# Kernel tuning notes

Hardware: AMD Instinct MI355X
Metric: run time of the kernel (lower is better)

The kernel has to match this reference:

```python
import jax, jax.numpy as jnp
import numpy as np

B, N, PHY, C, HID, FC, L, E = 2, 8192, 2, 64, 64, 128, 3, 524288

def _ln(x, g, b, eps=1e-5):
    mu = jnp.mean(x, axis=-1, keepdims=True)
    var = jnp.mean((x - mu) ** 2, axis=-1, keepdims=True)
    return (x - mu) * jax.lax.rsqrt(var + eps) * g + b

def setup_inputs() -> dict:
    key = jax.random.key(0)
    ks = jax.random.split(key, 24)
    s = 1.0 / np.sqrt(C)
    inp = {
        'x': jax.random.normal(ks[0], (B, N, 5), jnp.float32),
        'edge_index': jax.random.randint(ks[1], (2, E), 0, B * N, jnp.int32),
        'fc0_w': jax.random.normal(ks[2], (C, 4), jnp.float32) * 0.5,
        'fc0_b': jnp.zeros((C,), jnp.float32),
        'ln0_g': jnp.ones((C,), jnp.float32),
        'ln0_b': jnp.zeros((C,), jnp.float32),
        'gg_fc1_w': jax.random.normal(ks[3], (L, HID, C), jnp.float32) * s,
        'gg_fc1_b': jnp.zeros((L, HID), jnp.float32),
        'gg_fc2_w': jax.random.normal(ks[4], (L, C, HID), jnp.float32) * s,
        'gg_fc2_b': jnp.zeros((L, C), jnp.float32),
        'gg_weight': jax.random.uniform(ks[5], (L, HID), jnp.float32) + 0.5,
        'gg_freq': jax.random.normal(ks[6], (L, PHY, HID), jnp.float32) * (2 * np.pi),
        'wc_w': jax.random.normal(ks[7], (L, C, C), jnp.float32) * s,
        'wc_b': jnp.zeros((L, C), jnp.float32),
        'ln_g': jnp.ones((L, C), jnp.float32),
        'ln_b': jnp.zeros((L, C), jnp.float32),
        'fc1_w': jax.random.normal(ks[8], (FC, C), jnp.float32) * s,
        'fc1_b': jnp.zeros((FC,), jnp.float32),
        'fc2_w': jax.random.normal(ks[9], (1, FC), jnp.float32) / np.sqrt(FC),
        'fc2_b': jnp.zeros((1,), jnp.float32),
    }
    return inp

def reference(x, edge_index, fc0_w, fc0_b, ln0_g, ln0_b, gg_fc1_w, gg_fc1_b,
              gg_fc2_w, gg_fc2_b, gg_weight, gg_freq, wc_w, wc_b, ln_g, ln_b,
              fc1_w, fc1_b, fc2_w, fc2_b):
    grid = x[:, :, 2:4]           # (B,N,PHY): columns in_dim-phy_dim .. -1
    gw = x[:, :, 4]               # (B,N) grid_weight
    feat = x[:, :, :4]            # (B,N,in_dim)
    src, dst = edge_index[0], edge_index[1]
    grid_f = grid.reshape(-1, PHY)
    gw_f = gw.reshape(-1)
    vec = grid_f[src] - grid_f[dst]                      # (E,PHY)
    dist2 = jnp.sum(vec * vec, axis=-1, keepdims=True)   # (E,1)
    wgt_src = gw_f[src][:, None]                          # (E,1)

    h = feat @ fc0_w.T + fc0_b                            # (B,N,C)
    h = _ln(h, ln0_g, ln0_b)
    for l in range(L):
        w = gg_weight[l]                                  # (HID,)
        gauss = jnp.sqrt((w / jnp.pi) ** PHY) * jnp.exp(-w * dist2)  # (E,HID)
        fourier = jnp.sin(vec @ gg_freq[l])               # (E,HID)
        morlet = gauss * fourier
        hl = h @ gg_fc1_w[l].T + gg_fc1_b[l]              # (B,N,HID)
        val = morlet * hl.reshape(-1, HID)[src] * wgt_src # (E,HID)
        agg = jax.ops.segment_sum(val, dst, num_segments=B * N)
        x1 = agg.reshape(B, N, HID) @ gg_fc2_w[l].T + gg_fc2_b[l]
        x2 = h @ wc_w[l].T + wc_b[l]                      # pointwise Conv1d
        h = _ln(x1 + x2, ln_g[l], ln_b[l])
        if l != L - 1:
            h = jax.nn.gelu(h, approximate=False)
    h = jax.nn.gelu(h @ fc1_w.T + fc1_b, approximate=False)
    return h @ fc2_w.T + fc2_b                            # (B,N,1)
```

## Files before the change

### kernel.cpp

```cpp
#include <hip/hip_runtime.h>
#include <hip/hip_bf16.h>

#define M_NODES 16384
#define E_EDGES 524288
#define ASTR 68

typedef short short8 __attribute__((ext_vector_type(8)));
typedef float f32x4 __attribute__((ext_vector_type(4)));
typedef unsigned int uint4v __attribute__((ext_vector_type(4)));

#define PK_W1 0
#define PK_WC 12288
#define PK_W2 24576
#define PK_FC1 36864
#define PK_TOTAL 45056

static __device__ __forceinline__ float wredsum(float v) {
#pragma unroll
  for (int o = 32; o > 0; o >>= 1) v += __shfl_xor(v, o, 64);
  return v;
}

static __device__ __forceinline__ float gelu_exact(float x) {
  return 0.5f * x * (1.0f + erff(x * 0.70710678118654752440f));
}

static __device__ __forceinline__ unsigned int bsplit(float x) {
  unsigned int u = __float_as_uint(x);
  unsigned int hb = (u + 0x7FFFu + ((u >> 16) & 1u)) >> 16;
  float hf = __uint_as_float(hb << 16);
  float r = x - hf;
  unsigned int v = __float_as_uint(r);
  unsigned int lb = (v + 0x7FFFu + ((v >> 16) & 1u)) >> 16;
  return (hb & 0xFFFFu) | (lb << 16);
}

struct Frag { short8 hi, lo; };

static __device__ __forceinline__ Frag load_afrag(const unsigned int* a) {
  uint4v u0 = *(const uint4v*)a;
  uint4v u1 = *(const uint4v*)(a + 4);
  Frag f;
#pragma unroll
  for (int j = 0; j < 4; ++j) {
    f.hi[j]     = (short)(u0[j] & 0xFFFFu);
    f.lo[j]     = (short)(u0[j] >> 16);
    f.hi[j + 4] = (short)(u1[j] & 0xFFFFu);
    f.lo[j + 4] = (short)(u1[j] >> 16);
  }
  return f;
}

static __device__ __forceinline__ Frag load_bfrag(const float* __restrict__ w) {
  float4 w0 = *(const float4*)w;
  float4 w1 = *(const float4*)(w + 4);
  float v[8] = {w0.x, w0.y, w0.z, w0.w, w1.x, w1.y, w1.z, w1.w};
  Frag f;
#pragma unroll
  for (int j = 0; j < 8; ++j) {
    unsigned int p = bsplit(v[j]);
    f.hi[j] = (short)(p & 0xFFFFu);
    f.lo[j] = (short)(p >> 16);
  }
  return f;
}

static __device__ __forceinline__ f32x4 mfma3(const Frag& a, const Frag& b, f32x4 c) {
  c = __builtin_amdgcn_mfma_f32_16x16x32_bf16(a.hi, b.hi, c, 0, 0, 0);
  c = __builtin_amdgcn_mfma_f32_16x16x32_bf16(a.lo, b.hi, c, 0, 0, 0);
  c = __builtin_amdgcn_mfma_f32_16x16x32_bf16(a.hi, b.lo, c, 0, 0, 0);
  return c;
}

static __device__ __forceinline__ Frag load_bpk(const short* __restrict__ P, int S, int n, int off) {
  Frag f;
  f.hi = *(const short8*)(P + n * 64 + off);
  f.lo = *(const short8*)(P + S + n * 64 + off);
  return f;
}

__global__ __launch_bounds__(256) void k_front(
    const float* __restrict__ x,
    const float* __restrict__ fc0_w, const float* __restrict__ fc0_b,
    const float* __restrict__ ln0_g, const float* __restrict__ ln0_b,
    const float* __restrict__ gg_fc1_w, const float* __restrict__ gg_fc1_b,
    const float* __restrict__ wc_w, const float* __restrict__ wc_b,
    const float* __restrict__ gg_fc2_w, const float* __restrict__ fc1_w,
    const int* __restrict__ ei, int* __restrict__ cnt, short* __restrict__ pk,
    float2* __restrict__ grid2, float* __restrict__ gwf,
    float* __restrict__ hl, float* __restrict__ x2T)
{
  __shared__ unsigned int A[16 * ASTR];
  const int bid = blockIdx.x;
  const int tid = threadIdx.x;

  if (bid >= 3072) {
    int i = (bid - 3072) * 256 + tid;
    float v = (i < PK_WC)  ? gg_fc1_w[i]
            : (i < PK_W2)  ? wc_w[i - PK_WC]
            : (i < PK_FC1) ? gg_fc2_w[i - PK_W2]
                           : fc1_w[i - PK_FC1];
    int mb, sz;
    if (i < PK_FC1) { mb = i & ~4095; sz = 4096; } else { mb = PK_FC1; sz = 8192; }
    int k = i - mb;
    unsigned int p = bsplit(v);
    pk[2 * mb + k]      = (short)(p & 0xFFFFu);
    pk[2 * mb + sz + k] = (short)(p >> 16);
    return;
  }
  if (bid >= 1024) {
    int e = (bid - 1024) * 256 + tid;
    atomicAdd(&cnt[ei[E_EDGES + e]], 1);
    return;
  }

  const int lane = tid & 63, w = tid >> 6;
  const int tilebase = bid * 16;

  float fw0 = fc0_w[lane * 4 + 0], fw1 = fc0_w[lane * 4 + 1];
  float fw2v = fc0_w[lane * 4 + 2], fw3 = fc0_w[lane * 4 + 3];
  float fb = fc0_b[lane], g0 = ln0_g[lane], bb0 = ln0_b[lane];

#pragma unroll
  for (int i = 0; i < 4; ++i) {
    int node = tilebase + 4 * w + i;
    float xv0 = x[node * 5 + 0], xv1 = x[node * 5 + 1], xv2 = x[node * 5 + 2];
    float xv3 = x[node * 5 + 3], xv4 = x[node * 5 + 4];
    float acc = fb + xv0 * fw0 + xv1 * fw1 + xv2 * fw2v + xv3 * fw3;
    float mean = wredsum(acc) * (1.0f / 64.0f);
    float d = acc - mean;
    float var = wredsum(d * d) * (1.0f / 64.0f);
    float hv = d * rsqrtf(var + 1e-5f) * g0 + bb0;
    A[(4 * w + i) * ASTR + lane] = bsplit(hv);
    if (lane == 0) { grid2[node] = make_float2(xv2, xv3); gwf[node] = xv4; }
  }
  __syncthreads();

  const int c = lane & 15, q = lane >> 4;
  const int n = 16 * w + c;

  {
    Frag a0 = load_afrag(A + c * ASTR + 8 * q);
    Frag a1 = load_afrag(A + c * ASTR + 32 + 8 * q);
    Frag b0 = load_bfrag(gg_fc1_w + n * 64 + 8 * q);
    Frag b1 = load_bfrag(gg_fc1_w + n * 64 + 32 + 8 * q);
    f32x4 acc = {0.f, 0.f, 0.f, 0.f};
    acc = mfma3(a0, b0, acc);
    acc = mfma3(a1, b1, acc);
    float b1v = gg_fc1_b[n];
#pragma unroll
    for (int r = 0; r < 4; ++r)
      hl[(tilebase + 4 * q + r) * 64 + n] = acc[r] + b1v;

    Frag c0 = load_bfrag(wc_w + n * 64 + 8 * q);
    Frag c1 = load_bfrag(wc_w + n * 64 + 32 + 8 * q);
    f32x4 ac2 = {0.f, 0.f, 0.f, 0.f};
    ac2 = mfma3(a0, c0, ac2);
    ac2 = mfma3(a1, c1, ac2);
    float wcbv = wc_b[n];
    *(float4*)(x2T + n * M_NODES + tilebase + 4 * q) =
        make_float4(ac2[0] + wcbv, ac2[1] + wcbv, ac2[2] + wcbv, ac2[3] + wcbv);
  }
}

__global__ __launch_bounds__(1024) void k_scan(const int* __restrict__ cnt,
                                               int* __restrict__ row_start,
                                               int* __restrict__ cursor)
{
  const int PER = M_NODES / 1024;
  const int t = threadIdx.x;
  const int base = t * PER;
  int local[PER];
  int s = 0;
#pragma unroll
  for (int k = 0; k < PER; ++k) { local[k] = cnt[base + k]; s += local[k]; }

  __shared__ int part[1024];
  part[t] = s;
  __syncthreads();
  for (int off = 1; off < 1024; off <<= 1) {
    int v = (t >= off) ? part[t - off] : 0;
    __syncthreads();
    part[t] += v;
    __syncthreads();
  }
  int run = part[t] - s;
#pragma unroll
  for (int k = 0; k < PER; ++k) {
    row_start[base + k] = run;
    cursor[base + k] = run;
    run += local[k];
  }
  if (t == 1023) row_start[M_NODES] = run;
}

__global__ __launch_bounds__(256) void k_scatter(
    const int* __restrict__ ei, const float2* __restrict__ grid2,
    const float* __restrict__ gwf, int* __restrict__ cursor,
    float4* __restrict__ rec)
{
  int e = blockIdx.x * 256 + threadIdx.x;
  if (e < E_EDGES) {
    int s = ei[e];
    int dd = ei[E_EDGES + e];
    int pos = atomicAdd(&cursor[dd], 1);
    float2 gs = grid2[s], gd = grid2[dd];
    rec[pos] = make_float4(gs.x - gd.x, gs.y - gd.y, gwf[s], __int_as_float(s));
  }
}

#define EDGE_PHASE()                                                          \
  const float wv = gw[lane];                                                  \
  const float nwl2 = -wv * 1.44269504088896340736f;                           \
  const float lc = log2f(wv * 0.31830988618379067154f);                       \
  const float f0s = freq[lane] * 0.15915494309189533577f;                     \
  const float f1s = freq[64 + lane] * 0.15915494309189533577f;                \
  const float* hlp = hl_in + lane;                                            \
  for (int nn = 0; nn < 4; ++nn) {                                            \
    const int node = tilebase + 4 * w + nn;                                   \
    const int beg = row_start[node];                                          \
    const int cn = row_start[node + 1] - beg;                                 \
    float acc = 0.f;                                                          \
    if (cn > 0) {                                                             \
      float4 RA[8], RB[8]; float HA[8], HB[8];                                \
      auto ldg = [&](float4* R, float* H, int off) {                          \
        _Pragma("unroll")                                                     \
        for (int u = 0; u < 8; ++u) {                                         \
          int j = off + u; j = (j < cn) ? j : (cn - 1);                       \
          R[u] = rec[beg + j];                                                \
        }                                                                     \
        _Pragma("unroll")                                                     \
        for (int u = 0; u < 8; ++u)                                           \
          H[u] = hlp[__float_as_int(R[u].w) * 64];                            \
      };                                                                      \
      auto cmp8 = [&](const float4* R, const float* H, int off) {             \
        _Pragma("unroll")                                                     \
        for (int u = 0; u < 8; ++u) {                                         \
          if (off + u < cn) {                                                 \
            float dist2 = __builtin_fmaf(R[u].x, R[u].x, R[u].y * R[u].y);    \
            float gs = __builtin_amdgcn_exp2f(__builtin_fmaf(nwl2, dist2, lc));\
            float rev = __builtin_fmaf(R[u].x, f0s, R[u].y * f1s);            \
            float fo = __builtin_amdgcn_sinf(__builtin_amdgcn_fractf(rev));   \
            acc = __builtin_fmaf(gs * fo * H[u], R[u].z, acc);                \
          }                                                                   \
        }                                                                     \
      };                                                                      \
      const int Gp = (cn + 7) >> 3;                                           \
      ldg(RA, HA, 0);                                                         \
      int g = 0;                                                              \
      for (; g + 2 < Gp; g += 2) {                                            \
        ldg(RB, HB, 8 * (g + 1));                                             \
        cmp8(RA, HA, 8 * g);                                                  \
        ldg(RA, HA, 8 * (g + 2));                                             \
        cmp8(RB, HB, 8 * (g + 1));                                            \
      }                                                                       \
      if (g + 1 < Gp) {                                                       \
        ldg(RB, HB, 8 * (g + 1));                                             \
        cmp8(RA, HA, 8 * g);                                                  \
        cmp8(RB, HB, 8 * (g + 1));                                            \
      } else {                                                                \
        cmp8(RA, HA, 8 * g);                                                  \
      }                                                                       \
    }                                                                         \
    A[(4 * w + nn) * ASTR + lane] = bsplit(acc);                              \
  }

__global__ __launch_bounds__(256) void k_layer_mid(
    const float4* __restrict__ rec, const int* __restrict__ row_start,
    const float* __restrict__ hl_in,
    const float* __restrict__ gw, const float* __restrict__ freq,
    const short* __restrict__ pw2, const float* __restrict__ b2,
    const float* __restrict__ lng, const float* __restrict__ lnb,
    const short* __restrict__ pnw1, const float* __restrict__ nb1,
    const short* __restrict__ pnwc, const float* __restrict__ nwcb,
    float* __restrict__ hl_out, float* __restrict__ x2T)
{
  __shared__ unsigned int A[16 * ASTR];
  __shared__ float PS[4][16], PQ[4][16];
  const int tid = threadIdx.x, lane = tid & 63, w = tid >> 6;
  const int tilebase = blockIdx.x * 16;
  const int c = lane & 15, q = lane >> 4;
  const int n = 16 * w + c;

  float4 x2v = *(const float4*)(x2T + n * M_NODES + tilebase + 4 * q);
  float lg = lng[n], lb = lnb[n], vb = b2[n];
  float b1v = nb1[n], wcbv = nwcb[n];

  EDGE_PHASE()

  Frag wb0 = load_bpk(pw2, 4096, n, 8 * q);
  Frag wb1 = load_bpk(pw2, 4096, n, 32 + 8 * q);
  Frag n10 = load_bpk(pnw1, 4096, n, 8 * q);
  Frag n11 = load_bpk(pnw1, 4096, n, 32 + 8 * q);
  Frag nc0 = load_bpk(pnwc, 4096, n, 8 * q);
  Frag nc1 = load_bpk(pnwc, 4096, n, 32 + 8 * q);
  __syncthreads();

  Frag a0 = load_afrag(A + c * ASTR + 8 * q);
  Frag a1 = load_afrag(A + c * ASTR + 32 + 8 * q);
  f32x4 acc = {0.f, 0.f, 0.f, 0.f};
  acc = mfma3(a0, wb0, acc);
  acc = mfma3(a1, wb1, acc);

  float S[4];
#pragma unroll
  for (int r = 0; r < 4; ++r) S[r] = acc[r] + vb + x2v[r];

#pragma unroll
  for (int r = 0; r < 4; ++r) {
    float s1 = S[r], s2 = S[r] * S[r];
#pragma unroll
    for (int m = 1; m < 16; m <<= 1) {
      s1 += __shfl_xor(s1, m, 64);
      s2 += __shfl_xor(s2, m, 64);
    }
    if (c == 0) { PS[w][4 * q + r] = s1; PQ[w][4 * q + r] = s2; }
  }
  __syncthreads();

#pragma unroll
  for (int r = 0; r < 4; ++r) {
    int row = 4 * q + r;
    float sum = PS[0][row] + PS[1][row] + PS[2][row] + PS[3][row];
    float sq  = PQ[0][row] + PQ[1][row] + PQ[2][row] + PQ[3][row];
    float mean = sum * (1.0f / 64.0f);
    float var = sq * (1.0f / 64.0f) - mean * mean;
    float hv = (S[r] - mean) * rsqrtf(var + 1e-5f) * lg + lb;
    hv = gelu_exact(hv);
    A[row * ASTR + n] = bsplit(hv);
  }
  __syncthreads();

  Frag h0 = load_afrag(A + c * ASTR + 8 * q);
  Frag h1 = load_afrag(A + c * ASTR + 32 + 8 * q);

  f32x4 hh = {0.f, 0.f, 0.f, 0.f};
  hh = mfma3(h0, n10, hh);
  hh = mfma3(h1, n11, hh);
#pragma unroll
  for (int r = 0; r < 4; ++r)
    hl_out[(tilebase + 4 * q + r) * 64 + n] = hh[r] + b1v;

  f32x4 hx = {0.f, 0.f, 0.f, 0.f};
  hx = mfma3(h0, nc0, hx);
  hx = mfma3(h1, nc1, hx);
  *(float4*)(x2T + n * M_NODES + tilebase + 4 * q) =
      make_float4(hx[0] + wcbv, hx[1] + wcbv, hx[2] + wcbv, hx[3] + wcbv);
}

__global__ __launch_bounds__(256) void k_layer_last(
    const float4* __restrict__ rec, const int* __restrict__ row_start,
    const float* __restrict__ hl_in,
    const float* __restrict__ gw, const float* __restrict__ freq,
    const short* __restrict__ pw2, const float* __restrict__ b2,
    const float* __restrict__ lng, const float* __restrict__ lnb,
    const float* __restrict__ x2T,
    const short* __restrict__ pfc1, const float* __restrict__ fc1b,
    const float* __restrict__ fw2, const float* __restrict__ fb2,
    float* __restrict__ out)
{
  __shared__ unsigned int A[16 * ASTR];
  __shared__ float PS[4][16], PQ[4][16];
  const int tid = threadIdx.x, lane = tid & 63, w = tid >> 6;
  const int tilebase = blockIdx.x * 16;
  const int c = lane & 15, q = lane >> 4;
  const int n = 16 * w + c;

  float4 x2v = *(const float4*)(x2T + n * M_NODES + tilebase + 4 * q);
  float lg = lng[n], lb = lnb[n], vb = b2[n];

  EDGE_PHASE()

  Frag wb0 = load_bpk(pw2, 4096, n, 8 * q);
  Frag wb1 = load_bpk(pw2, 4096, n, 32 + 8 * q);
  __syncthreads();

  Frag a0 = load_afrag(A + c * ASTR + 8 * q);
  Frag a1 = load_afrag(A + c * ASTR + 32 + 8 * q);
  f32x4 acc = {0.f, 0.f, 0.f, 0.f};
  acc = mfma3(a0, wb0, acc);
  acc = mfma3(a1, wb1, acc);

  float S[4];
#pragma unroll
  for (int r = 0; r < 4; ++r) S[r] = acc[r] + vb + x2v[r];

#pragma unroll
  for (int r = 0; r < 4; ++r) {
    float s1 = S[r], s2 = S[r] * S[r];
#pragma unroll
    for (int m = 1; m < 16; m <<= 1) {
      s1 += __shfl_xor(s1, m, 64);
      s2 += __shfl_xor(s2, m, 64);
    }
    if (c == 0) { PS[w][4 * q + r] = s1; PQ[w][4 * q + r] = s2; }
  }
  __syncthreads();

#pragma unroll
  for (int r = 0; r < 4; ++r) {
    int row = 4 * q + r;
    float sum = PS[0][row] + PS[1][row] + PS[2][row] + PS[3][row];
    float sq  = PQ[0][row] + PQ[1][row] + PQ[2][row] + PQ[3][row];
    float mean = sum * (1.0f / 64.0f);
    float var = sq * (1.0f / 64.0f) - mean * mean;
    float hv = (S[r] - mean) * rsqrtf(var + 1e-5f) * lg + lb;
    A[row * ASTR + n] = bsplit(hv);
  }
  __syncthreads();

  Frag ha0 = load_afrag(A + c * ASTR + 8 * q);
  Frag ha1 = load_afrag(A + c * ASTR + 32 + 8 * q);
  float p[4] = {0.f, 0.f, 0.f, 0.f};
#pragma unroll
  for (int half = 0; half < 2; ++half) {
    int row = 32 * w + 16 * half + c;
    Frag b0 = load_bpk(pfc1, 8192, row, 8 * q);
    Frag b1 = load_bpk(pfc1, 8192, row, 32 + 8 * q);
    f32x4 a = {0.f, 0.f, 0.f, 0.f};
    a = mfma3(ha0, b0, a);
    a = mfma3(ha1, b1, a);
    float fbv = fc1b[row], fwv = fw2[row];
#pragma unroll
    for (int r = 0; r < 4; ++r) p[r] += gelu_exact(a[r] + fbv) * fwv;
  }
#pragma unroll
  for (int r = 0; r < 4; ++r) {
    float s = p[r];
#pragma unroll
    for (int m = 1; m < 16; m <<= 1) s += __shfl_xor(s, m, 64);
    if (c == 0) PS[w][4 * q + r] = s;
  }
  __syncthreads();
  if (tid < 16)
    out[tilebase + tid] = PS[0][tid] + PS[1][tid] + PS[2][tid] + PS[3][tid] + fb2[0];
}

extern "C" void kernel_launch(void* const* d_in, const int* in_sizes, int n_in,
                              void* d_out, int out_size, void* d_ws, size_t ws_size,
                              hipStream_t stream) {
  const float* x     = (const float*)d_in[0];
  const int* ei      = (const int*)d_in[1];
  const float* fc0_w = (const float*)d_in[2];
  const float* fc0_b = (const float*)d_in[3];
  const float* ln0_g = (const float*)d_in[4];
  const float* ln0_b = (const float*)d_in[5];
  const float* gg_fc1_w = (const float*)d_in[6];
  const float* gg_fc1_b = (const float*)d_in[7];
  const float* gg_fc2_w = (const float*)d_in[8];
  const float* gg_fc2_b = (const float*)d_in[9];
  const float* gg_weight = (const float*)d_in[10];
  const float* gg_freq   = (const float*)d_in[11];
  const float* wc_w = (const float*)d_in[12];
  const float* wc_b = (const float*)d_in[13];
  const float* ln_g = (const float*)d_in[14];
  const float* ln_b = (const float*)d_in[15];
  const float* fc1_w = (const float*)d_in[16];
  const float* fc1_b = (const float*)d_in[17];
  const float* fc2_w = (const float*)d_in[18];
  const float* fc2_b = (const float*)d_in[19];

  char* ws = (char*)d_ws;
  size_t off = 0;
  auto alloc = [&](size_t bytes) -> void* {
    void* p = ws + off;
    off = (off + bytes + 255) & ~(size_t)255;
    return p;
  };
  float2* grid2 = (float2*)alloc((size_t)M_NODES * 8);
  float*  gwf   = (float*)alloc((size_t)M_NODES * 4);
  float*  hl_a  = (float*)alloc((size_t)M_NODES * 64 * 4);
  float*  hl_b  = (float*)alloc((size_t)M_NODES * 64 * 4);
  float*  x2T   = (float*)alloc((size_t)M_NODES * 64 * 4);
  int*    cnt   = (int*)alloc((size_t)M_NODES * 4);
  int*    cursor= (int*)alloc((size_t)M_NODES * 4);
  int*    row_st= (int*)alloc((size_t)(M_NODES + 1) * 4);
  float4* rec   = (float4*)alloc((size_t)E_EDGES * 16);
  short*  pk    = (short*)alloc((size_t)PK_TOTAL * 2 * 2);
  (void)ws_size; (void)in_sizes; (void)n_in; (void)out_size;

  hipMemsetAsync(cnt, 0, (size_t)M_NODES * 4, stream);

  k_front<<<3248, 256, 0, stream>>>(x, fc0_w, fc0_b, ln0_g, ln0_b,
                                    gg_fc1_w, gg_fc1_b, wc_w, wc_b,
                                    gg_fc2_w, fc1_w,
                                    ei, cnt, pk, grid2, gwf, hl_a, x2T);
  k_scan<<<1, 1024, 0, stream>>>(cnt, row_st, cursor);
  k_scatter<<<E_EDGES / 256, 256, 0, stream>>>(ei, grid2, gwf, cursor, rec);

  k_layer_mid<<<M_NODES / 16, 256, 0, stream>>>(
      rec, row_st, hl_a, gg_weight + 0 * 64, gg_freq + 0 * 128,
      pk + 2 * (PK_W2 + 0 * 4096), gg_fc2_b + 0 * 64,
      ln_g + 0 * 64, ln_b + 0 * 64,
      pk + 2 * (PK_W1 + 1 * 4096), gg_fc1_b + 1 * 64,
      pk + 2 * (PK_WC + 1 * 4096), wc_b + 1 * 64,
      hl_b, x2T);
  k_layer_mid<<<M_NODES / 16, 256, 0, stream>>>(
      rec, row_st, hl_b, gg_weight + 1 * 64, gg_freq + 1 * 128,
      pk + 2 * (PK_W2 + 1 * 4096), gg_fc2_b + 1 * 64,
      ln_g + 1 * 64, ln_b + 1 * 64,
      pk + 2 * (PK_W1 + 2 * 4096), gg_fc1_b + 2 * 64,
      pk + 2 * (PK_WC + 2 * 4096), wc_b + 2 * 64,
      hl_a, x2T);
  k_layer_last<<<M_NODES / 16, 256, 0, stream>>>(
      rec, row_st, hl_a, gg_weight + 2 * 64, gg_freq + 2 * 128,
      pk + 2 * (PK_W2 + 2 * 4096), gg_fc2_b + 2 * 64,
      ln_g + 2 * 64, ln_b + 2 * 64,
      x2T,
      pk + 2 * PK_FC1, fc1_b, fc2_w, fc2_b,
      (float*)d_out);
}
```

Before: 263.5 us.

## Split edge records, prescale hl by source weight, broadcast edge data via readlane

The interleaved float4 edge record becomes two arrays: source indices and float2 displacement vectors. The per-source grid weight is folded into the stored hl features when they are produced, so it no longer has to be carried per edge. In the edge phase each wave loads up to 64 edges cooperatively, one per lane, and broadcasts each edge's data with readlane, replacing the earlier redundant per-lane loads of every record. This cuts edge-record bandwidth and wasted loads, at the cost of scalar readlane work and a sentinel element added to pad the edge arrays.

```diff
diff --git a/kernel.cpp b/kernel.cpp
--- a/kernel.cpp
+++ b/kernel.cpp
@@ -77,6 +77,10 @@
   f.hi = *(const short8*)(P + n * 64 + off);
   f.lo = *(const short8*)(P + S + n * 64 + off);
   return f;
+}
+
+static __device__ __forceinline__ float rdlanef(float v, int j) {
+  return __int_as_float(__builtin_amdgcn_readlane(__float_as_int(v), j));
 }
 
 __global__ __launch_bounds__(256) void k_front(
@@ -88,7 +92,7 @@
     const float* __restrict__ gg_fc2_w, const float* __restrict__ fc1_w,
     const int* __restrict__ ei, int* __restrict__ cnt, short* __restrict__ pk,
     float2* __restrict__ grid2, float* __restrict__ gwf,
-    float* __restrict__ hl, float* __restrict__ x2T)
+    float* __restrict__ hlf, float* __restrict__ x2T)
 {
   __shared__ unsigned int A[16 * ASTR];
   const int bid = blockIdx.x;
@@ -149,8 +153,10 @@
     acc = mfma3(a1, b1, acc);
     float b1v = gg_fc1_b[n];
 #pragma unroll
-    for (int r = 0; r < 4; ++r)
-      hl[(tilebase + 4 * q + r) * 64 + n] = acc[r] + b1v;
+    for (int r = 0; r < 4; ++r) {
+      float gwr = x[(tilebase + 4 * q + r) * 5 + 4];
+      hlf[(tilebase + 4 * q + r) * 64 + n] = (acc[r] + b1v) * gwr;
+    }
 
     Frag c0 = load_bfrag(wc_w + n * 64 + 8 * q);
     Frag c1 = load_bfrag(wc_w + n * 64 + 32 + 8 * q);
@@ -165,7 +171,9 @@
 
 __global__ __launch_bounds__(1024) void k_scan(const int* __restrict__ cnt,
                                                int* __restrict__ row_start,
-                                               int* __restrict__ cursor)
+                                               int* __restrict__ cursor,
+                                               int* __restrict__ esrc,
+                                               float2* __restrict__ evw)
 {
   const int PER = M_NODES / 1024;
   const int t = threadIdx.x;
@@ -192,12 +200,13 @@
     run += local[k];
   }
   if (t == 1023) row_start[M_NODES] = run;
+  if (t == 0) { esrc[E_EDGES] = 0; evw[E_EDGES] = make_float2(0.f, 0.f); }
 }
 
 __global__ __launch_bounds__(256) void k_scatter(
     const int* __restrict__ ei, const float2* __restrict__ grid2,
-    const float* __restrict__ gwf, int* __restrict__ cursor,
-    float4* __restrict__ rec)
+    int* __restrict__ cursor,
+    int* __restrict__ esrc, float2* __restrict__ evw)
 {
   int e = blockIdx.x * 256 + threadIdx.x;
   if (e < E_EDGES) {
@@ -205,7 +214,8 @@
     int dd = ei[E_EDGES + e];
     int pos = atomicAdd(&cursor[dd], 1);
     float2 gs = grid2[s], gd = grid2[dd];
-    rec[pos] = make_float4(gs.x - gd.x, gs.y - gd.y, gwf[s], __int_as_float(s));
+    esrc[pos] = s;
+    evw[pos] = make_float2(gs.x - gd.x, gs.y - gd.y);
   }
 }
 
@@ -215,65 +225,69 @@
   const float lc = log2f(wv * 0.31830988618379067154f);                       \
   const float f0s = freq[lane] * 0.15915494309189533577f;                     \
   const float f1s = freq[64 + lane] * 0.15915494309189533577f;                \
-  const float* hlp = hl_in + lane;                                            \
+  const float* __restrict__ hrow = hlf_in + lane;                             \
   for (int nn = 0; nn < 4; ++nn) {                                            \
     const int node = tilebase + 4 * w + nn;                                   \
     const int beg = row_start[node];                                          \
-    const int cn = row_start[node + 1] - beg;                                 \
+    const int end = row_start[node + 1];                                      \
     float acc = 0.f;                                                          \
-    if (cn > 0) {                                                             \
-      float4 RA[8], RB[8]; float HA[8], HB[8];                                \
-      auto ldg = [&](float4* R, float* H, int off) {                          \
+    for (int cb = beg; cb < end; cb += 64) {                                  \
+      const int cnc = min(64, end - cb);                                      \
+      const int idx = (lane < cnc) ? (cb + lane) : E_EDGES;                   \
+      const int src_l = esrc[idx];                                            \
+      const float2 v_l = evw[idx];                                            \
+      const float d2_l = __builtin_fmaf(v_l.x, v_l.x, v_l.y * v_l.y);         \
+      float HA[8], HB[8];                                                     \
+      auto g8 = [&](float* H, int g) {                                        \
         _Pragma("unroll")                                                     \
         for (int u = 0; u < 8; ++u) {                                         \
-          int j = off + u; j = (j < cn) ? j : (cn - 1);                       \
-          R[u] = rec[beg + j];                                                \
+          int ss = __builtin_amdgcn_readlane(src_l, 8 * g + u);               \
+          H[u] = hrow[(size_t)ss * 64];                                       \
         }                                                                     \
-        _Pragma("unroll")                                                     \
-        for (int u = 0; u < 8; ++u)                                           \
-          H[u] = hlp[__float_as_int(R[u].w) * 64];                            \
       };                                                                      \
-      auto cmp8 = [&](const float4* R, const float* H, int off) {             \
+      auto c8 = [&](const float* H, int g) {                                  \
         _Pragma("unroll")                                                     \
         for (int u = 0; u < 8; ++u) {                                         \
-          if (off + u < cn) {                                                 \
-            float dist2 = __builtin_fmaf(R[u].x, R[u].x, R[u].y * R[u].y);    \
-            float gs = __builtin_amdgcn_exp2f(__builtin_fmaf(nwl2, dist2, lc));\
-            float rev = __builtin_fmaf(R[u].x, f0s, R[u].y * f1s);            \
-            float fo = __builtin_amdgcn_sinf(__builtin_amdgcn_fractf(rev));   \
-            acc = __builtin_fmaf(gs * fo * H[u], R[u].z, acc);                \
-          }                                                                   \
+          int j = 8 * g + u;                                                  \
+          float svx = rdlanef(v_l.x, j);                                      \
+          float svy = rdlanef(v_l.y, j);                                      \
+          float sd2 = rdlanef(d2_l, j);                                       \
+          float ga = __builtin_amdgcn_exp2f(__builtin_fmaf(nwl2, sd2, lc));   \
+          float rv = __builtin_fmaf(svx, f0s, svy * f1s);                     \
+          float fo = __builtin_amdgcn_sinf(__builtin_amdgcn_fractf(rv));      \
+          acc = __builtin_fmaf(ga * fo, H[u], acc);                           \
         }                                                                     \
       };                                                                      \
-      const int Gp = (cn + 7) >> 3;                                           \
-      ldg(RA, HA, 0);                                                         \
+      const int Gp = (cnc + 7) >> 3;                                          \
+      g8(HA, 0);                                                              \
       int g = 0;                                                              \
       for (; g + 2 < Gp; g += 2) {                                            \
-        ldg(RB, HB, 8 * (g + 1));                                             \
-        cmp8(RA, HA, 8 * g);                                                  \
-        ldg(RA, HA, 8 * (g + 2));                                             \
-        cmp8(RB, HB, 8 * (g + 1));                                            \
+        g8(HB, g + 1);                                                        \
+        c8(HA, g);                                                            \
+        g8(HA, g + 2);                                                        \
+        c8(HB, g + 1);                                                        \
       }                                                                       \
       if (g + 1 < Gp) {                                                       \
-        ldg(RB, HB, 8 * (g + 1));                                             \
-        cmp8(RA, HA, 8 * g);                                                  \
-        cmp8(RB, HB, 8 * (g + 1));                                            \
+        g8(HB, g + 1);                                                        \
+        c8(HA, g);                                                            \
+        c8(HB, g + 1);                                                        \
       } else {                                                                \
-        cmp8(RA, HA, 8 * g);                                                  \
+        c8(HA, g);                                                            \
       }                                                                       \
     }                                                                         \
     A[(4 * w + nn) * ASTR + lane] = bsplit(acc);                              \
   }
 
 __global__ __launch_bounds__(256) void k_layer_mid(
-    const float4* __restrict__ rec, const int* __restrict__ row_start,
-    const float* __restrict__ hl_in,
+    const int* __restrict__ esrc, const float2* __restrict__ evw,
+    const int* __restrict__ row_start,
+    const float* __restrict__ hlf_in, const float* __restrict__ gwf,
     const float* __restrict__ gw, const float* __restrict__ freq,
     const short* __restrict__ pw2, const float* __restrict__ b2,
     const float* __restrict__ lng, const float* __restrict__ lnb,
     const short* __restrict__ pnw1, const float* __restrict__ nb1,
     const short* __restrict__ pnwc, const float* __restrict__ nwcb,
-    float* __restrict__ hl_out, float* __restrict__ x2T)
+    float* __restrict__ hlf_out, float* __restrict__ x2T)
 {
   __shared__ unsigned int A[16 * ASTR];
   __shared__ float PS[4][16], PQ[4][16];
@@ -283,6 +297,7 @@
   const int n = 16 * w + c;
 
   float4 x2v = *(const float4*)(x2T + n * M_NODES + tilebase + 4 * q);
+  float4 gw4 = *(const float4*)(gwf + tilebase + 4 * q);
   float lg = lng[n], lb = lnb[n], vb = b2[n];
   float b1v = nb1[n], wcbv = nwcb[n];
 
@@ -339,7 +354,7 @@
   hh = mfma3(h1, n11, hh);
 #pragma unroll
   for (int r = 0; r < 4; ++r)
-    hl_out[(tilebase + 4 * q + r) * 64 + n] = hh[r] + b1v;
+    hlf_out[(tilebase + 4 * q + r) * 64 + n] = (hh[r] + b1v) * gw4[r];
 
   f32x4 hx = {0.f, 0.f, 0.f, 0.f};
   hx = mfma3(h0, nc0, hx);
@@ -349,8 +364,9 @@
 }
 
 __global__ __launch_bounds__(256) void k_layer_last(
-    const float4* __restrict__ rec, const int* __restrict__ row_start,
-    const float* __restrict__ hl_in,
+    const int* __restrict__ esrc, const float2* __restrict__ evw,
+    const int* __restrict__ row_start,
+    const float* __restrict__ hlf_in,
     const float* __restrict__ gw, const float* __restrict__ freq,
     const short* __restrict__ pw2, const float* __restrict__ b2,
     const float* __restrict__ lng, const float* __restrict__ lnb,
@@ -469,13 +485,14 @@
   };
   float2* grid2 = (float2*)alloc((size_t)M_NODES * 8);
   float*  gwf   = (float*)alloc((size_t)M_NODES * 4);
-  float*  hl_a  = (float*)alloc((size_t)M_NODES * 64 * 4);
-  float*  hl_b  = (float*)alloc((size_t)M_NODES * 64 * 4);
+  float*  hlf_a = (float*)alloc((size_t)M_NODES * 64 * 4);
+  float*  hlf_b = (float*)alloc((size_t)M_NODES * 64 * 4);
   float*  x2T   = (float*)alloc((size_t)M_NODES * 64 * 4);
   int*    cnt   = (int*)alloc((size_t)M_NODES * 4);
   int*    cursor= (int*)alloc((size_t)M_NODES * 4);
   int*    row_st= (int*)alloc((size_t)(M_NODES + 1) * 4);
-  float4* rec   = (float4*)alloc((size_t)E_EDGES * 16);
+  int*    esrc  = (int*)alloc((size_t)(E_EDGES + 1) * 4);
+  float2* evw   = (float2*)alloc((size_t)(E_EDGES + 1) * 8);
   short*  pk    = (short*)alloc((size_t)PK_TOTAL * 2 * 2);
   (void)ws_size; (void)in_sizes; (void)n_in; (void)out_size;
 
@@ -484,26 +501,26 @@
   k_front<<<3248, 256, 0, stream>>>(x, fc0_w, fc0_b, ln0_g, ln0_b,
                                     gg_fc1_w, gg_fc1_b, wc_w, wc_b,
                                     gg_fc2_w, fc1_w,
-                                    ei, cnt, pk, grid2, gwf, hl_a, x2T);
-  k_scan<<<1, 1024, 0, stream>>>(cnt, row_st, cursor);
-  k_scatter<<<E_EDGES / 256, 256, 0, stream>>>(ei, grid2, gwf, cursor, rec);
+                                    ei, cnt, pk, grid2, gwf, hlf_a, x2T);
+  k_scan<<<1, 1024, 0, stream>>>(cnt, row_st, cursor, esrc, evw);
+  k_scatter<<<E_EDGES / 256, 256, 0, stream>>>(ei, grid2, cursor, esrc, evw);
 
   k_layer_mid<<<M_NODES / 16, 256, 0, stream>>>(
-      rec, row_st, hl_a, gg_weight + 0 * 64, gg_freq + 0 * 128,
+      esrc, evw, row_st, hlf_a, gwf, gg_weight + 0 * 64, gg_freq + 0 * 128,
       pk + 2 * (PK_W2 + 0 * 4096), gg_fc2_b + 0 * 64,
       ln_g + 0 * 64, ln_b + 0 * 64,
       pk + 2 * (PK_W1 + 1 * 4096), gg_fc1_b + 1 * 64,
       pk + 2 * (PK_WC + 1 * 4096), wc_b + 1 * 64,
-      hl_b, x2T);
+      hlf_b, x2T);
   k_layer_mid<<<M_NODES / 16, 256, 0, stream>>>(
-      rec, row_st, hl_b, gg_weight + 1 * 64, gg_freq + 1 * 128,
+      esrc, evw, row_st, hlf_b, gwf, gg_weight + 1 * 64, gg_freq + 1 * 128,
       pk + 2 * (PK_W2 + 1 * 4096), gg_fc2_b + 1 * 64,
       ln_g + 1 * 64, ln_b + 1 * 64,
       pk + 2 * (PK_W1 + 2 * 4096), gg_fc1_b + 2 * 64,
       pk + 2 * (PK_WC + 2 * 4096), wc_b + 2 * 64,
-      hl_a, x2T);
+      hlf_a, x2T);
   k_layer_last<<<M_NODES / 16, 256, 0, stream>>>(
-      rec, row_st, hl_a, gg_weight + 2 * 64, gg_freq + 2 * 128,
+      esrc, evw, row_st, hlf_a, gg_weight + 2 * 64, gg_freq + 2 * 128,
       pk + 2 * (PK_W2 + 2 * 4096), gg_fc2_b + 2 * 64,
       ln_g + 2 * 64, ln_b + 2 * 64,
       x2T,
```

Result: faster. 251.9 us (-4.4%).
